# Kernel optimization log

Hardware: AMD Instinct MI355X
Metric: run time of the kernel (lower is better)

The kernel has to match this reference:

```python
import jax, jax.numpy as jnp
import numpy as np

B, F0, D = 4096, 39, 16
CIN = [128, 128, 128]


def setup_inputs() -> dict:
    key = jax.random.key(0)
    ks = jax.random.split(key, 4)
    x = jax.random.normal(ks[0], (B, F0, D), dtype=jnp.float32)
    fields = [F0] + CIN
    inp = {"embedded_features": x}
    for i in range(len(CIN)):
        cin = F0 * fields[i]
        cout = fields[i + 1]
        kw = jax.random.fold_in(ks[1], i)
        # Conv1d default init scale ~ 1/sqrt(fan_in)
        inp[f"W{i}"] = jax.random.normal(kw, (cout, cin), dtype=jnp.float32) / np.sqrt(cin)
        inp[f"b{i}"] = jnp.zeros((cout,), dtype=jnp.float32)
    return inp


def _cin_layer(X0, Xi, W, b):
    # Math identical to: outer_product [B,F0,Fi,D] -> reshape [B,F0*Fi,D] -> 1x1 Conv1d.
    # Conv1d(kernel=1) over the flattened F0*Fi channel dim is a contraction over (j,k):
    #   Xn[b,h,d] = sum_{j,k} W[h, j*Fi+k] * X0[b,j,d] * Xi[b,k,d] + b[h]
    H = W.shape[0]
    F0_, Fi = X0.shape[1], Xi.shape[1]
    Wr = W.reshape(H, F0_, Fi)
    return jnp.einsum('hjk,bjd,bkd->bhd', Wr, X0, Xi) + b[None, :, None]


def reference(embedded_features, W0, b0, W1, b1, W2, b2):
    X0 = embedded_features  # [B, F0, D]
    Ws = [(W0, b0), (W1, b1), (W2, b2)]
    Xi = X0
    res = []
    for W, b in Ws:
        Xi = _cin_layer(X0, Xi, W, b)  # [B, H_i, D]
        res.append(Xi.sum(axis=2))     # sum over embedding dim
    return jnp.concatenate(res, axis=1)  # [B, sum(cin_size)]
```

## Files before the change

### kernel.cpp

```cpp
#include <hip/hip_runtime.h>
#include <stdint.h>


#define NB_F0 39
#define NB_H  128
#define NB_B  4096

typedef float f32x4  __attribute__((ext_vector_type(4)));
typedef float f32x16 __attribute__((ext_vector_type(16)));
typedef short s16x8  __attribute__((ext_vector_type(8)));

__device__ __forceinline__ void dma16(const void* g, void* l) {
  __builtin_amdgcn_global_load_lds(
      (const __attribute__((address_space(1))) unsigned int*)g,
      (__attribute__((address_space(3))) unsigned int*)l, 16, 0, 0);
}

__device__ __forceinline__ unsigned short rne_bf16(float f) {
  union { float f; unsigned u; } v; v.f = f;
  return (unsigned short)((v.u + 0x7fffu + ((v.u >> 16) & 1u)) >> 16);
}
__device__ __forceinline__ float bf16_to_f32(unsigned short s) {
  union { unsigned u; float f; } v; v.u = ((unsigned)s) << 16;
  return v.f;
}

__global__ void prep_x0_kernel(const float* __restrict__ X0g,
                               unsigned short* __restrict__ X0T,
                               unsigned short* __restrict__ X0c) {
  const int b = blockIdx.x;
  const int t = threadIdx.x;
  {
    const int d  = t >> 4;
    const int k4 = (t & 15) << 2;
    unsigned short vv[4];
#pragma unroll
    for (int i = 0; i < 4; ++i) {
      const int k = k4 + i;
      vv[i] = (k < NB_F0) ? rne_bf16(X0g[(size_t)b * (NB_F0 * 16) + k * 16 + d])
                          : (unsigned short)0;
    }
    ushort4 pk; pk.x = vv[0]; pk.y = vv[1]; pk.z = vv[2]; pk.w = vv[3];
    *(ushort4*)&X0T[((size_t)b * 16 + d) * 64 + k4] = pk;
  }
  for (int idx = t; idx < NB_F0 * 16; idx += 256) {
    const int j = idx >> 4, pos = idx & 15;
    const int d = (pos & 3) | (((pos >> 3) & 1) << 2) | (((pos >> 2) & 1) << 3);
    X0c[(size_t)b * (NB_F0 * 16) + idx] =
        rne_bf16(X0g[(size_t)b * (NB_F0 * 16) + j * 16 + d]);
  }
}

__global__ void prep_w_kernel(const float* __restrict__ Wsrc,
                              unsigned short* __restrict__ Wdst,
                              int Fi, int kshift, int total) {
  int idx = blockIdx.x * 256 + threadIdx.x;
  if (idx >= total) return;
  const int i    = idx & 7;
  const int lane = (idx >> 3) & 63;
  const int c    = (idx >> 9) & ((1 << kshift) - 1);
  const int jt   = idx >> (9 + kshift);
  const int t    = jt & 3;
  const int j    = jt >> 2;
  const int h = t * 32 + (lane & 31);
  const int k = c * 16 + ((lane >> 5) << 3) + i;
  unsigned short v = 0;
  if (k < Fi) v = rne_bf16(Wsrc[(size_t)h * (NB_F0 * Fi) + j * Fi + k]);
  Wdst[idx] = v;
}

template <int FI_PAD, bool STORE_XN>
__global__ __launch_bounds__(256, 2) void cin_layer(
    const unsigned short* __restrict__ Wf,
    const unsigned short* __restrict__ XiT,
    const unsigned short* __restrict__ X0c,
    const float* __restrict__ bias,
    unsigned short* __restrict__ XnT,
    float* __restrict__ outp)
{
  constexpr int KPASS = FI_PAD / 64;
  constexpr int KC16  = FI_PAD / 16;
  constexpr int S     = NB_F0 * KPASS;

  __shared__ __attribute__((aligned(16))) unsigned short Wlds[2][2048];
  __shared__ __attribute__((aligned(16))) unsigned short x0s[32 * NB_F0 * 16];

  const int tid  = threadIdx.x;
  const int lane = tid & 63;
  const int wv   = tid >> 6;
  const int L    = lane >> 5;
  const int col  = lane & 31;
  const int ht   = blockIdx.x >> 7;
  const int bblk = (blockIdx.x & 127) * 32;
  const int bwave = bblk + wv * 8;

  auto dma_stage = [&](int s, int buf) {
    const int pass = (KPASS == 2 && s >= NB_F0) ? 1 : 0;
    const int j = s - pass * NB_F0;
    const unsigned short* src =
        Wf + (((size_t)(j * 4 + ht) * KC16) + pass * 4 + wv) * 512 + lane * 8;
    dma16(src, &Wlds[buf][wv * 512]);
  };

  {
    const unsigned short* src = X0c + (size_t)bblk * (NB_F0 * 16);
    for (int c = tid; c < (32 * NB_F0 * 16) / 8; c += 256)
      *(s16x8*)&x0s[c * 8] = *(const s16x8*)&src[c * 8];
  }
  dma_stage(0, 0);

  s16x8 af[4][4];
  auto load_af = [&](int pass) {
#pragma unroll
    for (int P = 0; P < 4; ++P) {
      const unsigned short* base = XiT +
          ((size_t)(bwave + 2 * P + (col >> 4)) * 16 + (col & 15)) * FI_PAD +
          pass * 64 + L * 8;
#pragma unroll
      for (int c = 0; c < 4; ++c) af[P][c] = *(const s16x8*)(base + c * 16);
    }
  };
  load_af(0);

  f32x16 Xacc[4], kZero;
#pragma unroll
  for (int r = 0; r < 16; ++r) kZero[r] = 0.f;
#pragma unroll
  for (int P = 0; P < 4; ++P) Xacc[P] = kZero;

  const int x0base = (wv * 8) * (NB_F0 * 16) + L * 8;

  for (int s = 0; s < S; ++s) {
    __syncthreads();
    if (s + 1 < S) dma_stage(s + 1, (s + 1) & 1);
    if (KPASS == 2 && s == NB_F0) load_af(1);

    const int j = (KPASS == 2 && s >= NB_F0) ? s - NB_F0 : s;
    const unsigned short* wb = &Wlds[s & 1][lane * 8];
    const s16x8 w0 = *(const s16x8*)(wb);
    const s16x8 w1 = *(const s16x8*)(wb + 512);
    const s16x8 w2 = *(const s16x8*)(wb + 1024);
    const s16x8 w3 = *(const s16x8*)(wb + 1536);

#pragma unroll
    for (int P = 0; P < 4; ++P) {
      f32x16 y;
      y = __builtin_amdgcn_mfma_f32_32x32x16_bf16(af[P][0], w0, kZero, 0, 0, 0);
      y = __builtin_amdgcn_mfma_f32_32x32x16_bf16(af[P][1], w1, y, 0, 0, 0);
      y = __builtin_amdgcn_mfma_f32_32x32x16_bf16(af[P][2], w2, y, 0, 0, 0);
      y = __builtin_amdgcn_mfma_f32_32x32x16_bf16(af[P][3], w3, y, 0, 0, 0);

      const uint4 xu0 = *(const uint4*)
          &x0s[x0base + (2 * P + 0) * (NB_F0 * 16) + j * 16];
      const uint4 xu1 = *(const uint4*)
          &x0s[x0base + (2 * P + 1) * (NB_F0 * 16) + j * 16];
      const unsigned wd[8] = {xu0.x, xu0.y, xu0.z, xu0.w,
                              xu1.x, xu1.y, xu1.z, xu1.w};
      f32x16 xsc;
#pragma unroll
      for (int i = 0; i < 8; ++i) {
        xsc[2 * i]     = __uint_as_float(wd[i] << 16);
        xsc[2 * i + 1] = __uint_as_float(wd[i] & 0xffff0000u);
      }
      Xacc[P] = __builtin_elementwise_fma(xsc, y, Xacc[P]);
    }
  }

  const float bias_v = bias[ht * 32 + col];
#pragma unroll
  for (int P = 0; P < 4; ++P) {
#pragma unroll
    for (int bh = 0; bh < 2; ++bh) {
      const int b = bwave + 2 * P + bh;
      float v[8];
#pragma unroll
      for (int m = 0; m < 8; ++m) v[m] = Xacc[P][bh * 8 + m] + bias_v;
      if (STORE_XN) {
#pragma unroll
        for (int m = 0; m < 8; ++m) {
          const int d = (m & 3) + 8 * ((m >> 2) & 1) + 4 * L;
          XnT[((size_t)b * 16 + d) * NB_H + ht * 32 + col] = rne_bf16(v[m]);
        }
      }
      float tot = ((v[0] + v[1]) + (v[2] + v[3])) + ((v[4] + v[5]) + (v[6] + v[7]));
      tot += __shfl_xor(tot, 32);
      if (lane < 32) outp[(size_t)b * 384 + ht * 32 + lane] = tot;
    }
  }
}

extern "C" void kernel_launch(void* const* d_in, const int* in_sizes, int n_in,
                              void* d_out, int out_size, void* d_ws, size_t ws_size,
                              hipStream_t stream) {
  (void)in_sizes; (void)n_in; (void)out_size; (void)ws_size;
  const float* X0g = (const float*)d_in[0];
  const float* W0  = (const float*)d_in[1];
  const float* b0  = (const float*)d_in[2];
  const float* W1  = (const float*)d_in[3];
  const float* b1  = (const float*)d_in[4];
  const float* W2  = (const float*)d_in[5];
  const float* b2  = (const float*)d_in[6];
  float* out = (float*)d_out;

  char* p = (char*)d_ws;
  unsigned short* X0T = (unsigned short*)p; p += (size_t)NB_B * 16 * 64 * 2;
  unsigned short* X0c = (unsigned short*)p; p += (size_t)NB_B * NB_F0 * 16 * 2;
  unsigned short* X1T = (unsigned short*)p; p += (size_t)NB_B * 16 * 128 * 2;
  unsigned short* X2T = (unsigned short*)p; p += (size_t)NB_B * 16 * 128 * 2;
  unsigned short* Wf0 = (unsigned short*)p; p += (size_t)NB_F0 * 4 * 4 * 512 * 2;
  unsigned short* Wf1 = (unsigned short*)p; p += (size_t)NB_F0 * 4 * 8 * 512 * 2;
  unsigned short* Wf2 = (unsigned short*)p; p += (size_t)NB_F0 * 4 * 8 * 512 * 2;

  hipLaunchKernelGGL(prep_x0_kernel, dim3(NB_B), dim3(256), 0, stream,
                     X0g, X0T, X0c);
  const int tw0  = NB_F0 * 4 * 4 * 512;
  const int tw12 = NB_F0 * 4 * 8 * 512;
  hipLaunchKernelGGL(prep_w_kernel, dim3((tw0 + 255) / 256), dim3(256), 0, stream,
                     W0, Wf0, 39, 2, tw0);
  hipLaunchKernelGGL(prep_w_kernel, dim3((tw12 + 255) / 256), dim3(256), 0, stream,
                     W1, Wf1, 128, 3, tw12);
  hipLaunchKernelGGL(prep_w_kernel, dim3((tw12 + 255) / 256), dim3(256), 0, stream,
                     W2, Wf2, 128, 3, tw12);

  hipLaunchKernelGGL((cin_layer<64, true>),   dim3(512), dim3(256), 0, stream,
                     Wf0, X0T, X0c, b0, X1T, out + 0);
  hipLaunchKernelGGL((cin_layer<128, true>),  dim3(512), dim3(256), 0, stream,
                     Wf1, X1T, X0c, b1, X2T, out + 128);
  hipLaunchKernelGGL((cin_layer<128, false>), dim3(512), dim3(256), 0, stream,
                     Wf2, X2T, X0c, b2, (unsigned short*)nullptr, out + 256);
}
```

Measured before the change: 310.7 us.

## Load weight fragments directly into registers with double-buffered prefetch instead of LDS DMA

Removes the LDS staging buffer for weights and the per-step __syncthreads. Each wave now loads its own weight fragments from global memory straight into registers, and a two-set register ping-pong prefetches the next step while the current one computes. This drops the block-wide barrier and the LDS round trip from the main loop. The cost is that all four waves fetch the same weight fragments redundantly (served from L1/L2) and register pressure rises, which could hurt occupancy under launch_bounds(256,2).

```diff
diff --git a/kernel.cpp b/kernel.cpp
--- a/kernel.cpp
+++ b/kernel.cpp
@@ -9,12 +9,6 @@
 typedef float f32x4  __attribute__((ext_vector_type(4)));
 typedef float f32x16 __attribute__((ext_vector_type(16)));
 typedef short s16x8  __attribute__((ext_vector_type(8)));
-
-__device__ __forceinline__ void dma16(const void* g, void* l) {
-  __builtin_amdgcn_global_load_lds(
-      (const __attribute__((address_space(1))) unsigned int*)g,
-      (__attribute__((address_space(3))) unsigned int*)l, 16, 0, 0);
-}
 
 __device__ __forceinline__ unsigned short rne_bf16(float f) {
   union { float f; unsigned u; } v; v.f = f;
@@ -82,7 +76,6 @@
   constexpr int KC16  = FI_PAD / 16;
   constexpr int S     = NB_F0 * KPASS;
 
-  __shared__ __attribute__((aligned(16))) unsigned short Wlds[2][2048];
   __shared__ __attribute__((aligned(16))) unsigned short x0s[32 * NB_F0 * 16];
 
   const int tid  = threadIdx.x;
@@ -94,20 +87,11 @@
   const int bblk = (blockIdx.x & 127) * 32;
   const int bwave = bblk + wv * 8;
 
-  auto dma_stage = [&](int s, int buf) {
-    const int pass = (KPASS == 2 && s >= NB_F0) ? 1 : 0;
-    const int j = s - pass * NB_F0;
-    const unsigned short* src =
-        Wf + (((size_t)(j * 4 + ht) * KC16) + pass * 4 + wv) * 512 + lane * 8;
-    dma16(src, &Wlds[buf][wv * 512]);
-  };
-
   {
     const unsigned short* src = X0c + (size_t)bblk * (NB_F0 * 16);
     for (int c = tid; c < (32 * NB_F0 * 16) / 8; c += 256)
       *(s16x8*)&x0s[c * 8] = *(const s16x8*)&src[c * 8];
   }
-  dma_stage(0, 0);
 
   s16x8 af[4][4];
   auto load_af = [&](int pass) {
@@ -128,43 +112,64 @@
 #pragma unroll
   for (int P = 0; P < 4; ++P) Xacc[P] = kZero;
 
+  __syncthreads();
+
   const int x0base = (wv * 8) * (NB_F0 * 16) + L * 8;
 
-  for (int s = 0; s < S; ++s) {
-    __syncthreads();
-    if (s + 1 < S) dma_stage(s + 1, (s + 1) & 1);
+  const s16x8* __restrict__ Wf8 = (const s16x8*)Wf;
+  auto wload = [&](int s, s16x8 (&w)[4]) {
+    const int pass = (KPASS == 2 && s >= NB_F0) ? 1 : 0;
+    const int j = s - pass * NB_F0;
+    const s16x8* p = Wf8 + ((j * 4 + ht) * KC16 + pass * 4) * 64 + lane;
+#pragma unroll
+    for (int cc = 0; cc < 4; ++cc) w[cc] = p[cc * 64];
+  };
+
+  auto compute = [&](int s, const s16x8 (&w)[4]) {
     if (KPASS == 2 && s == NB_F0) load_af(1);
-
     const int j = (KPASS == 2 && s >= NB_F0) ? s - NB_F0 : s;
-    const unsigned short* wb = &Wlds[s & 1][lane * 8];
-    const s16x8 w0 = *(const s16x8*)(wb);
-    const s16x8 w1 = *(const s16x8*)(wb + 512);
-    const s16x8 w2 = *(const s16x8*)(wb + 1024);
-    const s16x8 w3 = *(const s16x8*)(wb + 1536);
-
+    const unsigned short* xr = &x0s[x0base + j * 16];
 #pragma unroll
     for (int P = 0; P < 4; ++P) {
       f32x16 y;
-      y = __builtin_amdgcn_mfma_f32_32x32x16_bf16(af[P][0], w0, kZero, 0, 0, 0);
-      y = __builtin_amdgcn_mfma_f32_32x32x16_bf16(af[P][1], w1, y, 0, 0, 0);
-      y = __builtin_amdgcn_mfma_f32_32x32x16_bf16(af[P][2], w2, y, 0, 0, 0);
-      y = __builtin_amdgcn_mfma_f32_32x32x16_bf16(af[P][3], w3, y, 0, 0, 0);
-
-      const uint4 xu0 = *(const uint4*)
-          &x0s[x0base + (2 * P + 0) * (NB_F0 * 16) + j * 16];
-      const uint4 xu1 = *(const uint4*)
-          &x0s[x0base + (2 * P + 1) * (NB_F0 * 16) + j * 16];
-      const unsigned wd[8] = {xu0.x, xu0.y, xu0.z, xu0.w,
-                              xu1.x, xu1.y, xu1.z, xu1.w};
+      y = __builtin_amdgcn_mfma_f32_32x32x16_bf16(af[P][0], w[0], kZero, 0, 0, 0);
+      y = __builtin_amdgcn_mfma_f32_32x32x16_bf16(af[P][1], w[1], y, 0, 0, 0);
+      y = __builtin_amdgcn_mfma_f32_32x32x16_bf16(af[P][2], w[2], y, 0, 0, 0);
+      y = __builtin_amdgcn_mfma_f32_32x32x16_bf16(af[P][3], w[3], y, 0, 0, 0);
+
+      const uint4 xu0 = *(const uint4*)(xr + (2 * P + 0) * (NB_F0 * 16));
+      const uint4 xu1 = *(const uint4*)(xr + (2 * P + 1) * (NB_F0 * 16));
       f32x16 xsc;
-#pragma unroll
-      for (int i = 0; i < 8; ++i) {
-        xsc[2 * i]     = __uint_as_float(wd[i] << 16);
-        xsc[2 * i + 1] = __uint_as_float(wd[i] & 0xffff0000u);
-      }
+      xsc[0]  = __uint_as_float(xu0.x << 16);
+      xsc[1]  = __uint_as_float(xu0.x & 0xffff0000u);
+      xsc[2]  = __uint_as_float(xu0.y << 16);
+      xsc[3]  = __uint_as_float(xu0.y & 0xffff0000u);
+      xsc[4]  = __uint_as_float(xu0.z << 16);
+      xsc[5]  = __uint_as_float(xu0.z & 0xffff0000u);
+      xsc[6]  = __uint_as_float(xu0.w << 16);
+      xsc[7]  = __uint_as_float(xu0.w & 0xffff0000u);
+      xsc[8]  = __uint_as_float(xu1.x << 16);
+      xsc[9]  = __uint_as_float(xu1.x & 0xffff0000u);
+      xsc[10] = __uint_as_float(xu1.y << 16);
+      xsc[11] = __uint_as_float(xu1.y & 0xffff0000u);
+      xsc[12] = __uint_as_float(xu1.z << 16);
+      xsc[13] = __uint_as_float(xu1.z & 0xffff0000u);
+      xsc[14] = __uint_as_float(xu1.w << 16);
+      xsc[15] = __uint_as_float(xu1.w & 0xffff0000u);
       Xacc[P] = __builtin_elementwise_fma(xsc, y, Xacc[P]);
     }
-  }
+  };
+
+  s16x8 wA[4], wB[4];
+  wload(0, wA);
+  int s = 0;
+  for (; s + 2 <= S; s += 2) {
+    wload(s + 1, wB);
+    compute(s, wA);
+    if (s + 2 < S) wload(s + 2, wA);
+    compute(s + 1, wB);
+  }
+  if (s < S) compute(s, wA);
 
   const float bias_v = bias[ht * 32 + col];
 #pragma unroll
```

Result: slower. 374.5 us (+20.5%).
